# Kernel optimization log

Hardware: AMD Instinct MI355X
Metric: run time of the kernel (lower is better)

Reference implementation:

```python
import jax, jax.numpy as jnp
import numpy as np

NUM_CLASSES = 21
THRESH = 0.5
NEG_POS = 3
VAR0, VAR1 = 0.1, 0.2  # SSD cfg['variance']
B, P, O = 32, 32768, 50


def point_form(boxes):
    # center form (cx,cy,w,h) -> corner form (xmin,ymin,xmax,ymax)
    return jnp.concatenate([boxes[:, :2] - boxes[:, 2:] / 2,
                            boxes[:, :2] + boxes[:, 2:] / 2], axis=1)


def jaccard(box_a, box_b):
    # box_a [A,4], box_b [B,4], corner form -> IoU [A,B]
    max_xy = jnp.minimum(box_a[:, None, 2:], box_b[None, :, 2:])
    min_xy = jnp.maximum(box_a[:, None, :2], box_b[None, :, :2])
    inter = jnp.prod(jnp.clip(max_xy - min_xy, 0.0, None), axis=2)
    area_a = jnp.prod(box_a[:, 2:] - box_a[:, :2], axis=1)[:, None]
    area_b = jnp.prod(box_b[:, 2:] - box_b[:, :2], axis=1)[None, :]
    return inter / (area_a + area_b - inter)


def encode(matched, priors):
    # matched corner form [P,4], priors center form [P,4]
    g_cxcy = ((matched[:, :2] + matched[:, 2:]) / 2 - priors[:, :2]) / (VAR0 * priors[:, 2:])
    g_wh = jnp.log((matched[:, 2:] - matched[:, :2]) / priors[:, 2:]) / VAR1
    return jnp.concatenate([g_cxcy, g_wh], axis=1)


def match_one(truths, labels, priors):
    # truths [O,4] corner, labels [O], priors [P,4] center
    overlaps = jaccard(truths, point_form(priors))          # [O,P]
    best_prior_idx = jnp.argmax(overlaps, axis=1)           # [O]
    best_truth_overlap = jnp.max(overlaps, axis=0)          # [P]
    best_truth_idx = jnp.argmax(overlaps, axis=0)           # [P]
    # ensure every gt matches its best prior
    best_truth_overlap = best_truth_overlap.at[best_prior_idx].set(2.0)
    best_truth_idx = best_truth_idx.at[best_prior_idx].set(jnp.arange(truths.shape[0]))
    matches = truths[best_truth_idx]                        # [P,4]
    conf = (labels[best_truth_idx] + 1.0).astype(jnp.int32)
    conf = jnp.where(best_truth_overlap < THRESH, 0, conf)
    return encode(matches, priors), conf


def setup_inputs() -> dict:
    key = jax.random.key(0)
    k1, k2, k3, k4, k5, k6 = jax.random.split(key, 6)
    loc_data = jax.random.normal(k1, (B, P, 4), dtype=jnp.float32)
    conf_data = jax.random.normal(k2, (B, P, NUM_CLASSES), dtype=jnp.float32)
    # priors in center form: centers in (0,1), sizes in (0.02, 0.5)
    cxy = jax.random.uniform(k3, (P, 2), dtype=jnp.float32)
    wh = jax.random.uniform(k4, (P, 2), dtype=jnp.float32, minval=0.02, maxval=0.5)
    priors = jnp.concatenate([cxy, wh], axis=1)
    # targets: valid corner-form boxes + label
    pts = jax.random.uniform(k5, (B, O, 2, 2), dtype=jnp.float32)
    xymin = pts.min(axis=2)
    xymax = jnp.maximum(pts.max(axis=2), xymin + 0.01)
    labels = jax.random.randint(k6, (B, O), 0, NUM_CLASSES - 1).astype(jnp.float32)
    targets = jnp.concatenate([xymin, xymax, labels[..., None]], axis=-1)
    return {"loc_data": loc_data, "conf_data": conf_data, "priors": priors, "targets": targets}


def reference(loc_data, conf_data, priors, targets):
    truths = targets[..., :4]
    labels = targets[..., 4]
    loc_t, conf_t = jax.vmap(match_one, in_axes=(0, 0, None))(truths, labels, priors)
    loc_t = jax.lax.stop_gradient(loc_t)
    conf_t = jax.lax.stop_gradient(conf_t)

    pos = conf_t > 0                                         # [B,P]
    # localization: smooth-L1, summed over positives
    diff = loc_data - loc_t
    ad = jnp.abs(diff)
    sl1 = jnp.where(ad < 1.0, 0.5 * diff * diff, ad - 0.5)
    loss_l = jnp.sum(sl1 * pos[..., None].astype(sl1.dtype))

    # per-prior softmax CE (logsumexp - true logit)
    lse = jax.nn.logsumexp(conf_data, axis=-1)               # [B,P]
    true_logit = jnp.take_along_axis(conf_data, conf_t[..., None], axis=-1)[..., 0]
    ce = lse - true_logit                                    # [B,P]

    # hard negative mining: rank negatives by CE (pos zeroed out)
    ce_mine = jnp.where(pos, 0.0, ce)
    loss_idx = jnp.argsort(-ce_mine, axis=1)
    idx_rank = jnp.argsort(loss_idx, axis=1)
    num_pos = jnp.sum(pos, axis=1, keepdims=True)            # [B,1]
    num_neg = jnp.clip(NEG_POS * num_pos, None, pos.shape[1] - 1)
    neg = idx_rank < num_neg

    sel = pos | neg
    loss_c = jnp.sum(jnp.where(sel, ce, 0.0))

    N = jnp.sum(num_pos).astype(loss_l.dtype)
    return loss_l / N, loss_c / N
```

## Files before the change

### kernel.cpp

```cpp
#include <hip/hip_runtime.h>
#include <math.h>

#define BB 32
#define PP 32768
#define OO 50
#define NT 25
#define NC 21
#define MPT 4

#define WBINLO (104 << 7)
#define WBINS  2048

typedef unsigned long long u64;
typedef unsigned int u32;
typedef unsigned char u8;

static constexpr u32 HALF_BITS = 0x3F000000u;

static constexpr size_t OFF_WHC   = 0;
static constexpr size_t OFF_WHS   = OFF_WHC  + 4ull*BB*WBINS;
static constexpr size_t OFF_KEYS  = OFF_WHS  + 4ull*BB*WBINS;
static constexpr size_t OFF_NPOS  = OFF_KEYS + 8ull*BB*OO;
static constexpr size_t OFF_DACC  = OFF_NPOS + 128;
static constexpr size_t ZERO_BYTES = OFF_DACC + 8ull*3*BB;
static constexpr size_t OFF_KEY2  = ((ZERO_BYTES + 127) & ~127ull);

__global__ __launch_bounds__(256) void zero_kernel(ulonglong2* __restrict__ dst, size_t n16) {
    size_t i = (size_t)blockIdx.x * 256 + threadIdx.x;
    if (i < n16) dst[i] = make_ulonglong2(0ull, 0ull);
}

static __device__ __forceinline__ float fast_div(float a, float b) {
    return a * __builtin_amdgcn_rcpf(b);
}

__global__ __launch_bounds__(256) void match_kernel(
    const float* __restrict__ priors, const float* __restrict__ targets,
    u64* __restrict__ key2, u64* __restrict__ keys)
{
#pragma clang fp contract(off)
    const int b = blockIdx.y;
    const int half = blockIdx.z;
    const int obase = half * NT;
    const int tid = threadIdx.x;
    const int lane = tid & 63, wid = tid >> 6;
    const int wbase = blockIdx.x * (256 * MPT) + wid * (64 * MPT);

    __shared__ float tr[NT * 5];
    __shared__ u64 wkeys[4][NT];
    if (tid < NT * 5) tr[tid] = targets[(size_t)b * OO * 5 + obase * 5 + tid];
    __syncthreads();

    float px1[MPT], py1[MPT], px2[MPT], py2[MPT], area_p[MPT];
#pragma unroll
    for (int s = 0; s < MPT; ++s) {
        int p = wbase + s * 64 + lane;
        float4 pr = *(const float4*)(priors + (size_t)p * 4);
        px1[s] = pr.x - pr.z * 0.5f; py1[s] = pr.y - pr.w * 0.5f;
        px2[s] = pr.x + pr.z * 0.5f; py2[s] = pr.y + pr.w * 0.5f;
        area_p[s] = (px2[s] - px1[s]) * (py2[s] - py1[s]);
    }

    float bestv[MPT]; int besto[MPT];
#pragma unroll
    for (int s = 0; s < MPT; ++s) { bestv[s] = -1.0f; besto[s] = 0; }

    for (int o = 0; o < NT; ++o) {
        float tx1 = tr[o*5+0], ty1 = tr[o*5+1], tx2 = tr[o*5+2], ty2 = tr[o*5+3];
        float area_t = (tx2 - tx1) * (ty2 - ty1);
        float iou[MPT];
#pragma unroll
        for (int s = 0; s < MPT; ++s) {
            float ix1 = fmaxf(tx1, px1[s]), iy1 = fmaxf(ty1, py1[s]);
            float ix2 = fminf(tx2, px2[s]), iy2 = fminf(ty2, py2[s]);
            float dx = fmaxf(ix2 - ix1, 0.0f), dy = fmaxf(iy2 - iy1, 0.0f);
            float inter = dx * dy;
            iou[s] = fast_div(inter, (area_t + area_p[s]) - inter);
            if (iou[s] > bestv[s]) { bestv[s] = iou[s]; besto[s] = o; }
        }
        float mv = fmaxf(fmaxf(iou[0], iou[1]), fmaxf(iou[2], iou[3]));
        for (int m = 1; m < 64; m <<= 1)
            mv = fmaxf(mv, __shfl_xor(mv, m, 64));
        u64 b0 = __ballot(iou[0] == mv);
        u64 b1 = __ballot(iou[1] == mv);
        u64 b2 = __ballot(iou[2] == mv);
        u64 b3 = __ballot(iou[3] == mv);
        if (lane == 0) {
            int s, l;
            if      (b0) { s = 0; l = __ffsll(b0) - 1; }
            else if (b1) { s = 1; l = __ffsll(b1) - 1; }
            else if (b2) { s = 2; l = __ffsll(b2) - 1; }
            else if (b3) { s = 3; l = __ffsll(b3) - 1; }
            else         { s = 0; l = 0; }
            u32 wp = (u32)(wbase + s * 64 + l);
            wkeys[wid][o] = ((u64)__float_as_uint(mv) << 32) | (u64)(0xFFFFFFFFu - wp);
        }
    }
#pragma unroll
    for (int s = 0; s < MPT; ++s) {
        int p = wbase + s * 64 + lane;
        u64 key = ((u64)__float_as_uint(bestv[s]) << 32)
                | (u64)(u32)(49 - (obase + besto[s]));
        key2[((size_t)half * BB + b) * PP + p] = key;
    }
    __syncthreads();
    if (tid < NT) {
        u64 k0 = wkeys[0][tid];
        for (int w = 1; w < 4; ++w) { u64 kw = wkeys[w][tid]; if (kw > k0) k0 = kw; }
        atomicMax(&keys[b * OO + obase + tid], k0);
    }
}

static __device__ __forceinline__ u32 top16bits(float v) {
    u32 u = __float_as_uint(v);
    return (v > 0.0f) ? u : 0u;
}

static __device__ __forceinline__ u64 umax64(u64 a, u64 b) { return a > b ? a : b; }

#define EL(k) ((((k) & 3) == 0) ? v[(k) >> 2].x : \
               (((k) & 3) == 1) ? v[(k) >> 2].y : \
               (((k) & 3) == 2) ? v[(k) >> 2].z : v[(k) >> 2].w)

__global__ __launch_bounds__(256) void score_kernel(
    const float* __restrict__ loc, const float* __restrict__ conf,
    const float* __restrict__ priors, const float* __restrict__ targets,
    const u64* __restrict__ key2, const u64* __restrict__ keys,
    int* __restrict__ npos, double* __restrict__ dacc,
    u32* __restrict__ whc, float* __restrict__ whs)
{
    const int b = blockIdx.y;
    const int tid = threadIdx.x;
    const int p = blockIdx.x * 1024 + tid * 4;
    __shared__ float tr[OO * 5];
    __shared__ u32 fp[OO];
    __shared__ __align__(16) u32 hh[WBINS];
    __shared__ __align__(16) float hs[WBINS];
    if (tid < OO * 5) tr[tid] = targets[(size_t)b * OO * 5 + tid];
    if (tid < OO) fp[tid] = 0xFFFFFFFFu - (u32)(keys[b * OO + tid] & 0xFFFFFFFFull);
#pragma unroll
    for (int j = 0; j < WBINS / 256; ++j) { hh[j * 256 + tid] = 0; hs[j * 256 + tid] = 0.0f; }
    __syncthreads();

    ulonglong2 a01 = *(const ulonglong2*)(key2 + (size_t)b * PP + p);
    ulonglong2 a23 = *(const ulonglong2*)(key2 + (size_t)b * PP + p + 2);
    ulonglong2 c01 = *(const ulonglong2*)(key2 + ((size_t)BB + b) * PP + p);
    ulonglong2 c23 = *(const ulonglong2*)(key2 + ((size_t)BB + b) * PP + p + 2);
    const u64 kk[4] = {umax64(a01.x, c01.x), umax64(a01.y, c01.y),
                       umax64(a23.x, c23.x), umax64(a23.y, c23.y)};

    int fo[4] = {-1, -1, -1, -1};
    for (int o = 0; o < OO; ++o) {
        u32 fpo = fp[o];
#pragma unroll
        for (int r = 0; r < 4; ++r) if (fpo == (u32)(p + r)) fo[r] = o;
    }

    const float4* cp = (const float4*)(conf + ((size_t)b * PP + p) * NC);
    float4 v[21];
    float cev[4];
    double l_l = 0.0, pce = 0.0; int np_ = 0;

#pragma unroll
    for (int r = 0; r < 4; ++r) {
        const int jlo = (r == 0) ? 0 : ((21 * (r - 1) + 20) / 4 + 1);
        const int jhi = (21 * r + 20) / 4;
#pragma unroll
        for (int j = jlo; j <= jhi; ++j) v[j] = cp[j];

        const u32 hi = (u32)(kk[r] >> 32);
        const u32 lo = (u32)kk[r];
        const bool forced = fo[r] >= 0;
        const int o = forced ? fo[r] : (int)(49u - lo);
        const bool pos = forced || hi >= HALF_BITS;
        const int conft = pos ? (int)(tr[o * 5 + 4] + 1.0f) : 0;

        float m = -1e30f;
#pragma unroll
        for (int c = 0; c < NC; ++c) m = fmaxf(m, EL(21 * r + c));
        float s = 0.0f, tl = 0.0f;
#pragma unroll
        for (int c = 0; c < NC; ++c) {
            float xx = EL(21 * r + c);
            s += expf(xx - m);
            if (c == conft) tl = xx;
        }
        float ce = (m + logf(s)) - tl;
        cev[r] = pos ? 0.0f : ce;

        if (pos) {
            np_ += 1; pce += (double)ce;
            float mx1 = tr[o*5+0], my1 = tr[o*5+1], mx2 = tr[o*5+2], my2 = tr[o*5+3];
            float4 pr = *(const float4*)(priors + (size_t)(p + r) * 4);
            float lt0 = ((mx1 + mx2) * 0.5f - pr.x) / (0.1f * pr.z);
            float lt1 = ((my1 + my2) * 0.5f - pr.y) / (0.1f * pr.w);
            float lt2 = logf((mx2 - mx1) / pr.z) / 0.2f;
            float lt3 = logf((my2 - my1) / pr.w) / 0.2f;
            float4 l4 = *(const float4*)(loc + ((size_t)b * PP + p + r) * 4);
            float lpv[4] = {l4.x, l4.y, l4.z, l4.w};
            float lt[4] = {lt0, lt1, lt2, lt3};
#pragma unroll
            for (int i2 = 0; i2 < 4; ++i2) {
                float d = lpv[i2] - lt[i2];
                float ad = fabsf(d);
                l_l += (double)(ad < 1.0f ? 0.5f * d * d : ad - 0.5f);
            }
        }
    }

#pragma unroll
    for (int r = 0; r < 4; ++r) {
        u32 t16 = top16bits(cev[r]) >> 16;
        if (t16 != 0) {
            int widx = ((int)t16 - WBINLO) >> 1;
            widx = widx < 0 ? 0 : (widx > WBINS - 1 ? WBINS - 1 : widx);
            atomicAdd(&hh[widx], 1u);
            atomicAdd(&hs[widx], cev[r]);
        }
    }
    __syncthreads();
#pragma unroll
    for (int j = 0; j < WBINS / 256; ++j) {
        u32 c = hh[j * 256 + tid];
        if (c) {
            atomicAdd(&whc[(size_t)b * WBINS + j * 256 + tid], c);
            atomicAdd(&whs[(size_t)b * WBINS + j * 256 + tid], hs[j * 256 + tid]);
        }
    }
    __syncthreads();
    double* rl = (double*)hh;
    double* rc = (double*)hs;
    int*    rn = (int*)(hh + 1024);
    rl[tid] = l_l; rc[tid] = pce; rn[tid] = np_;
    __syncthreads();
    for (int s2 = 128; s2 > 0; s2 >>= 1) {
        if (tid < s2) { rl[tid] += rl[tid+s2]; rc[tid] += rc[tid+s2]; rn[tid] += rn[tid+s2]; }
        __syncthreads();
    }
    if (tid == 0) {
        atomicAdd(&dacc[b], rl[0]);
        atomicAdd(&dacc[BB + b], rc[0]);
        atomicAdd(&npos[b], rn[0]);
    }
}

__global__ __launch_bounds__(256) void selwin_kernel(
    const u32* __restrict__ whc, const float* __restrict__ whs,
    const int* __restrict__ npos, double* __restrict__ dacc)
{
    const int b = blockIdx.x, tid = threadIdx.x;
    const int lane = tid & 63, wid = tid >> 6;
    int k = npos[b] * 3; if (k > PP - 1) k = PP - 1;
    if (k <= 0) return;
    const u32* hc = whc + (size_t)b * WBINS;
    const float* hsg = whs + (size_t)b * WBINS;

    __shared__ u32 ccnt_[WBINS / 256]; __shared__ float csum_[WBINS / 256];
    __shared__ u32 ct[256]; __shared__ float fs[256];
    __shared__ int s_cT; __shared__ u32 s_aboveC; __shared__ float s_aboveS;
    __shared__ u32 sT;

    for (int c = wid; c < WBINS / 256; c += 4) {
        u32 cnt = 0; float sm = 0.0f;
#pragma unroll
        for (int q = 0; q < 4; ++q) {
            int idx = c * 256 + q * 64 + lane;
            cnt += hc[idx];
            sm  += hsg[idx];
        }
        for (int m = 1; m < 64; m <<= 1) {
            cnt += __shfl_xor(cnt, m, 64);
            sm  += __shfl_xor(sm, m, 64);
        }
        if (lane == 0) { ccnt_[c] = cnt; csum_[c] = sm; }
    }
    if (tid == 0) sT = 0;
    __syncthreads();
    if (tid == 0) {
        u32 cum = 0; float scum = 0.0f; int cT = -1; u32 aboveC = 0; float aboveS = 0.0f;
        for (int c = WBINS / 256 - 1; c >= 0; --c) {
            if (cum + ccnt_[c] >= (u32)k) { cT = c; aboveC = cum; aboveS = scum; break; }
            cum += ccnt_[c]; scum += csum_[c];
        }
        s_cT = cT; s_aboveC = aboveC; s_aboveS = aboveS;
        if (cT < 0) dacc[2 * BB + b] = (double)scum;
    }
    __syncthreads();
    const int cT = s_cT;
    if (cT < 0) return;
    const u32 aboveC = s_aboveC; const float aboveS = s_aboveS;

    const u32 myc = hc[cT * 256 + tid];
    const float mys = hsg[cT * 256 + tid];
    ct[tid] = myc; fs[tid] = mys;
    __syncthreads();
    for (int off = 1; off < 256; off <<= 1) {
        u32 a1 = (tid + off < 256) ? ct[tid + off] : 0;
        float a2 = (tid + off < 256) ? fs[tid + off] : 0.0f;
        __syncthreads();
        ct[tid] += a1; fs[tid] += a2;
        __syncthreads();
    }
    if (aboveC + ct[tid] >= (u32)k) atomicMax(&sT, (u32)tid);
    __syncthreads();
    const int T = (int)sT;
    if (tid == T) {
        u32 aboveBinC = aboveC + ((T < 255) ? ct[T + 1] : 0);
        float aboveBinS = aboveS + ((T < 255) ? fs[T + 1] : 0.0f);
        int k2 = k - (int)aboveBinC;
        double avg = (double)mys / (double)myc;
        dacc[2 * BB + b] = (double)aboveBinS + (double)k2 * avg;
    }
}

__global__ void finalize_kernel(const int* __restrict__ npos,
                                const double* __restrict__ dacc, float* __restrict__ out) {
    if (threadIdx.x == 0 && blockIdx.x == 0) {
        double N = 0.0, ll = 0.0, lc = 0.0;
        for (int b = 0; b < BB; ++b) {
            N += (double)npos[b];
            ll += dacc[b];
            lc += dacc[BB + b] + dacc[2 * BB + b];
        }
        out[0] = (float)(ll / N);
        out[1] = (float)(lc / N);
    }
}

extern "C" void kernel_launch(void* const* d_in, const int* in_sizes, int n_in,
                              void* d_out, int out_size, void* d_ws, size_t ws_size,
                              hipStream_t stream) {
    const float* loc     = (const float*)d_in[0];
    const float* conf    = (const float*)d_in[1];
    const float* priors  = (const float*)d_in[2];
    const float* targets = (const float*)d_in[3];
    char* ws = (char*)d_ws;
    u32*    whc   = (u32*)   (ws + OFF_WHC);
    float*  whs   = (float*) (ws + OFF_WHS);
    u64*    keys  = (u64*)   (ws + OFF_KEYS);
    int*    npos  = (int*)   (ws + OFF_NPOS);
    double* dacc  = (double*)(ws + OFF_DACC);
    u64*    key2  = (u64*)   (ws + OFF_KEY2);
    float*  out   = (float*)d_out;

    const size_t n16 = ZERO_BYTES / 16;
    zero_kernel<<<(unsigned)((n16 + 255) / 256), 256, 0, stream>>>((ulonglong2*)ws, n16);
    match_kernel<<<dim3(PP / (256 * MPT), BB, 2), 256, 0, stream>>>(priors, targets, key2, keys);
    score_kernel<<<dim3(PP / 1024, BB), 256, 0, stream>>>(loc, conf, priors, targets, key2, keys, npos, dacc, whc, whs);
    selwin_kernel<<<BB, 256, 0, stream>>>(whc, whs, npos, dacc);
    finalize_kernel<<<1, 64, 0, stream>>>(npos, dacc, out);
}
```

Before: 98.62 us.

## Fuse zeroing into match, replace atomics with partials, merge tail kernels

```diff
diff --git a/kernel.cpp b/kernel.cpp
--- a/kernel.cpp
+++ b/kernel.cpp
@@ -6,71 +6,73 @@
 #define OO 50
 #define NT 25
 #define NC 21
-#define MPT 4
 
 #define WBINLO (104 << 7)
 #define WBINS  2048
 
 typedef unsigned long long u64;
 typedef unsigned int u32;
-typedef unsigned char u8;
 
 static constexpr u32 HALF_BITS = 0x3F000000u;
 
 static constexpr size_t OFF_WHC   = 0;
 static constexpr size_t OFF_WHS   = OFF_WHC  + 4ull*BB*WBINS;
-static constexpr size_t OFF_KEYS  = OFF_WHS  + 4ull*BB*WBINS;
-static constexpr size_t OFF_NPOS  = OFF_KEYS + 8ull*BB*OO;
+static constexpr size_t OFF_NPOS  = OFF_WHS  + 4ull*BB*WBINS;
 static constexpr size_t OFF_DACC  = OFF_NPOS + 128;
 static constexpr size_t ZERO_BYTES = OFF_DACC + 8ull*3*BB;
-static constexpr size_t OFF_KEY2  = ((ZERO_BYTES + 127) & ~127ull);
-
-__global__ __launch_bounds__(256) void zero_kernel(ulonglong2* __restrict__ dst, size_t n16) {
-    size_t i = (size_t)blockIdx.x * 256 + threadIdx.x;
-    if (i < n16) dst[i] = make_ulonglong2(0ull, 0ull);
-}
+static constexpr size_t OFF_KPART = ((ZERO_BYTES + 127) & ~127ull);
+static constexpr size_t OFF_KEY2  = OFF_KPART + 8ull*BB*OO*64;
 
 static __device__ __forceinline__ float fast_div(float a, float b) {
     return a * __builtin_amdgcn_rcpf(b);
 }
+static __device__ __forceinline__ u32 top16bits(float v) {
+    u32 u = __float_as_uint(v);
+    return (v > 0.0f) ? u : 0u;
+}
+static __device__ __forceinline__ u64 umax64(u64 a, u64 b) { return a > b ? a : b; }
 
 __global__ __launch_bounds__(256) void match_kernel(
     const float* __restrict__ priors, const float* __restrict__ targets,
-    u64* __restrict__ key2, u64* __restrict__ keys)
+    u64* __restrict__ key2, u64* __restrict__ kpart, ulonglong2* __restrict__ zbase)
 {
-#pragma clang fp contract(off)
     const int b = blockIdx.y;
     const int half = blockIdx.z;
     const int obase = half * NT;
     const int tid = threadIdx.x;
     const int lane = tid & 63, wid = tid >> 6;
-    const int wbase = blockIdx.x * (256 * MPT) + wid * (64 * MPT);
+    const int chunk = blockIdx.x;
+    const int p = chunk * 1024 + tid * 4;
+
+    if (b == 0 && half == 0) {
+        for (size_t i = (size_t)chunk * 256 + tid; i < ZERO_BYTES / 16; i += 32 * 256)
+            zbase[i] = make_ulonglong2(0ull, 0ull);
+    }
 
     __shared__ float tr[NT * 5];
     __shared__ u64 wkeys[4][NT];
     if (tid < NT * 5) tr[tid] = targets[(size_t)b * OO * 5 + obase * 5 + tid];
     __syncthreads();
 
-    float px1[MPT], py1[MPT], px2[MPT], py2[MPT], area_p[MPT];
-#pragma unroll
-    for (int s = 0; s < MPT; ++s) {
-        int p = wbase + s * 64 + lane;
-        float4 pr = *(const float4*)(priors + (size_t)p * 4);
+    float px1[4], py1[4], px2[4], py2[4], area_p[4];
+#pragma unroll
+    for (int s = 0; s < 4; ++s) {
+        float4 pr = *(const float4*)(priors + (size_t)(p + s) * 4);
         px1[s] = pr.x - pr.z * 0.5f; py1[s] = pr.y - pr.w * 0.5f;
         px2[s] = pr.x + pr.z * 0.5f; py2[s] = pr.y + pr.w * 0.5f;
         area_p[s] = (px2[s] - px1[s]) * (py2[s] - py1[s]);
     }
 
-    float bestv[MPT]; int besto[MPT];
-#pragma unroll
-    for (int s = 0; s < MPT; ++s) { bestv[s] = -1.0f; besto[s] = 0; }
+    float bestv[4]; int besto[4];
+#pragma unroll
+    for (int s = 0; s < 4; ++s) { bestv[s] = -1.0f; besto[s] = 0; }
 
     for (int o = 0; o < NT; ++o) {
         float tx1 = tr[o*5+0], ty1 = tr[o*5+1], tx2 = tr[o*5+2], ty2 = tr[o*5+3];
         float area_t = (tx2 - tx1) * (ty2 - ty1);
-        float iou[MPT];
-#pragma unroll
-        for (int s = 0; s < MPT; ++s) {
+        float iou[4];
+#pragma unroll
+        for (int s = 0; s < 4; ++s) {
             float ix1 = fmaxf(tx1, px1[s]), iy1 = fmaxf(ty1, py1[s]);
             float ix2 = fminf(tx2, px2[s]), iy2 = fminf(ty2, py2[s]);
             float dx = fmaxf(ix2 - ix1, 0.0f), dy = fmaxf(iy2 - iy1, 0.0f);
@@ -78,45 +80,35 @@
             iou[s] = fast_div(inter, (area_t + area_p[s]) - inter);
             if (iou[s] > bestv[s]) { bestv[s] = iou[s]; besto[s] = o; }
         }
-        float mv = fmaxf(fmaxf(iou[0], iou[1]), fmaxf(iou[2], iou[3]));
+        float tmax = iou[0]; int ts = 0;
+#pragma unroll
+        for (int s = 1; s < 4; ++s) if (iou[s] > tmax) { tmax = iou[s]; ts = s; }
+        float mv = tmax;
         for (int m = 1; m < 64; m <<= 1)
             mv = fmaxf(mv, __shfl_xor(mv, m, 64));
-        u64 b0 = __ballot(iou[0] == mv);
-        u64 b1 = __ballot(iou[1] == mv);
-        u64 b2 = __ballot(iou[2] == mv);
-        u64 b3 = __ballot(iou[3] == mv);
-        if (lane == 0) {
-            int s, l;
-            if      (b0) { s = 0; l = __ffsll(b0) - 1; }
-            else if (b1) { s = 1; l = __ffsll(b1) - 1; }
-            else if (b2) { s = 2; l = __ffsll(b2) - 1; }
-            else if (b3) { s = 3; l = __ffsll(b3) - 1; }
-            else         { s = 0; l = 0; }
-            u32 wp = (u32)(wbase + s * 64 + l);
-            wkeys[wid][o] = ((u64)__float_as_uint(mv) << 32) | (u64)(0xFFFFFFFFu - wp);
-        }
-    }
-#pragma unroll
-    for (int s = 0; s < MPT; ++s) {
-        int p = wbase + s * 64 + lane;
-        u64 key = ((u64)__float_as_uint(bestv[s]) << 32)
-                | (u64)(u32)(49 - (obase + besto[s]));
-        key2[((size_t)half * BB + b) * PP + p] = key;
+        u64 bm = __ballot(tmax == mv);
+        if (lane == (int)(__ffsll((long long)bm) - 1))
+            wkeys[wid][o] = ((u64)__float_as_uint(mv) << 32)
+                          | (u64)(0xFFFFFFFFu - (u32)(p + ts));
+    }
+
+    {
+        u64 k0 = ((u64)__float_as_uint(bestv[0]) << 32) | (u64)(u32)(49 - (obase + besto[0]));
+        u64 k1 = ((u64)__float_as_uint(bestv[1]) << 32) | (u64)(u32)(49 - (obase + besto[1]));
+        u64 k2 = ((u64)__float_as_uint(bestv[2]) << 32) | (u64)(u32)(49 - (obase + besto[2]));
+        u64 k3 = ((u64)__float_as_uint(bestv[3]) << 32) | (u64)(u32)(49 - (obase + besto[3]));
+        u64* dst = key2 + ((size_t)half * BB + b) * PP + p;
+        *(ulonglong2*)dst = make_ulonglong2(k0, k1);
+        *(ulonglong2*)(dst + 2) = make_ulonglong2(k2, k3);
     }
     __syncthreads();
     if (tid < NT) {
         u64 k0 = wkeys[0][tid];
-        for (int w = 1; w < 4; ++w) { u64 kw = wkeys[w][tid]; if (kw > k0) k0 = kw; }
-        atomicMax(&keys[b * OO + obase + tid], k0);
-    }
-}
-
-static __device__ __forceinline__ u32 top16bits(float v) {
-    u32 u = __float_as_uint(v);
-    return (v > 0.0f) ? u : 0u;
-}
-
-static __device__ __forceinline__ u64 umax64(u64 a, u64 b) { return a > b ? a : b; }
+#pragma unroll
+        for (int w = 1; w < 4; ++w) k0 = umax64(k0, wkeys[w][tid]);
+        kpart[((size_t)b * OO + obase + tid) * 64 + chunk * 2 + half] = k0;
+    }
+}
 
 #define EL(k) ((((k) & 3) == 0) ? v[(k) >> 2].x : \
                (((k) & 3) == 1) ? v[(k) >> 2].y : \
@@ -125,7 +117,7 @@
 __global__ __launch_bounds__(256) void score_kernel(
     const float* __restrict__ loc, const float* __restrict__ conf,
     const float* __restrict__ priors, const float* __restrict__ targets,
-    const u64* __restrict__ key2, const u64* __restrict__ keys,
+    const u64* __restrict__ key2, const u64* __restrict__ kpart,
     int* __restrict__ npos, double* __restrict__ dacc,
     u32* __restrict__ whc, float* __restrict__ whs)
 {
@@ -137,7 +129,12 @@
     __shared__ __align__(16) u32 hh[WBINS];
     __shared__ __align__(16) float hs[WBINS];
     if (tid < OO * 5) tr[tid] = targets[(size_t)b * OO * 5 + tid];
-    if (tid < OO) fp[tid] = 0xFFFFFFFFu - (u32)(keys[b * OO + tid] & 0xFFFFFFFFull);
+    if (tid < OO) {
+        const u64* kp = kpart + ((size_t)b * OO + tid) * 64;
+        u64 k0 = kp[0];
+        for (int c = 1; c < 64; ++c) k0 = umax64(k0, kp[c]);
+        fp[tid] = 0xFFFFFFFFu - (u32)(k0 & 0xFFFFFFFFull);
+    }
 #pragma unroll
     for (int j = 0; j < WBINS / 256; ++j) { hh[j * 256 + tid] = 0; hs[j * 256 + tid] = 0.0f; }
     __syncthreads();
@@ -244,78 +241,79 @@
     }
 }
 
-__global__ __launch_bounds__(256) void selwin_kernel(
+__global__ __launch_bounds__(256) void tail_kernel(
     const u32* __restrict__ whc, const float* __restrict__ whs,
-    const int* __restrict__ npos, double* __restrict__ dacc)
+    const int* __restrict__ npos, double* __restrict__ dacc,
+    float* __restrict__ out)
 {
-    const int b = blockIdx.x, tid = threadIdx.x;
+    const int tid = threadIdx.x;
     const int lane = tid & 63, wid = tid >> 6;
-    int k = npos[b] * 3; if (k > PP - 1) k = PP - 1;
-    if (k <= 0) return;
-    const u32* hc = whc + (size_t)b * WBINS;
-    const float* hsg = whs + (size_t)b * WBINS;
-
     __shared__ u32 ccnt_[WBINS / 256]; __shared__ float csum_[WBINS / 256];
     __shared__ u32 ct[256]; __shared__ float fs[256];
     __shared__ int s_cT; __shared__ u32 s_aboveC; __shared__ float s_aboveS;
     __shared__ u32 sT;
 
-    for (int c = wid; c < WBINS / 256; c += 4) {
-        u32 cnt = 0; float sm = 0.0f;
-#pragma unroll
-        for (int q = 0; q < 4; ++q) {
-            int idx = c * 256 + q * 64 + lane;
-            cnt += hc[idx];
-            sm  += hsg[idx];
-        }
-        for (int m = 1; m < 64; m <<= 1) {
-            cnt += __shfl_xor(cnt, m, 64);
-            sm  += __shfl_xor(sm, m, 64);
-        }
-        if (lane == 0) { ccnt_[c] = cnt; csum_[c] = sm; }
-    }
-    if (tid == 0) sT = 0;
+    for (int b = 0; b < BB; ++b) {
+        int k = npos[b] * 3; if (k > PP - 1) k = PP - 1;
+        if (k > 0) {
+            const u32* hc = whc + (size_t)b * WBINS;
+            const float* hsg = whs + (size_t)b * WBINS;
+            for (int c = wid; c < WBINS / 256; c += 4) {
+                u32 cnt = 0; float sm = 0.0f;
+#pragma unroll
+                for (int q = 0; q < 4; ++q) {
+                    int idx = c * 256 + q * 64 + lane;
+                    cnt += hc[idx];
+                    sm  += hsg[idx];
+                }
+                for (int m = 1; m < 64; m <<= 1) {
+                    cnt += __shfl_xor(cnt, m, 64);
+                    sm  += __shfl_xor(sm, m, 64);
+                }
+                if (lane == 0) { ccnt_[c] = cnt; csum_[c] = sm; }
+            }
+            if (tid == 0) sT = 0;
+            __syncthreads();
+            if (tid == 0) {
+                u32 cum = 0; float scum = 0.0f; int cT = -1; u32 aC = 0; float aS = 0.0f;
+                for (int c = WBINS / 256 - 1; c >= 0; --c) {
+                    if (cum + ccnt_[c] >= (u32)k) { cT = c; aC = cum; aS = scum; break; }
+                    cum += ccnt_[c]; scum += csum_[c];
+                }
+                s_cT = cT; s_aboveC = aC; s_aboveS = aS;
+                if (cT < 0) dacc[2 * BB + b] = (double)scum;
+            }
+            __syncthreads();
+            const int cT = s_cT;
+            if (cT >= 0) {
+                const u32 aboveC = s_aboveC; const float aboveS = s_aboveS;
+                const u32 myc = hc[cT * 256 + tid];
+                const float mys = hsg[cT * 256 + tid];
+                ct[tid] = myc; fs[tid] = mys;
+                __syncthreads();
+                for (int off = 1; off < 256; off <<= 1) {
+                    u32 a1 = (tid + off < 256) ? ct[tid + off] : 0;
+                    float a2 = (tid + off < 256) ? fs[tid + off] : 0.0f;
+                    __syncthreads();
+                    ct[tid] += a1; fs[tid] += a2;
+                    __syncthreads();
+                }
+                if (aboveC + ct[tid] >= (u32)k) atomicMax(&sT, (u32)tid);
+                __syncthreads();
+                const int T = (int)sT;
+                if (tid == T) {
+                    u32 aboveBinC = aboveC + ((T < 255) ? ct[T + 1] : 0);
+                    float aboveBinS = aboveS + ((T < 255) ? fs[T + 1] : 0.0f);
+                    int k2 = k - (int)aboveBinC;
+                    double avg = (double)mys / (double)myc;
+                    dacc[2 * BB + b] = (double)aboveBinS + (double)k2 * avg;
+                }
+            }
+            __syncthreads();
+        }
+    }
     __syncthreads();
     if (tid == 0) {
-        u32 cum = 0; float scum = 0.0f; int cT = -1; u32 aboveC = 0; float aboveS = 0.0f;
-        for (int c = WBINS / 256 - 1; c >= 0; --c) {
-            if (cum + ccnt_[c] >= (u32)k) { cT = c; aboveC = cum; aboveS = scum; break; }
-            cum += ccnt_[c]; scum += csum_[c];
-        }
-        s_cT = cT; s_aboveC = aboveC; s_aboveS = aboveS;
-        if (cT < 0) dacc[2 * BB + b] = (double)scum;
-    }
-    __syncthreads();
-    const int cT = s_cT;
-    if (cT < 0) return;
-    const u32 aboveC = s_aboveC; const float aboveS = s_aboveS;
-
-    const u32 myc = hc[cT * 256 + tid];
-    const float mys = hsg[cT * 256 + tid];
-    ct[tid] = myc; fs[tid] = mys;
-    __syncthreads();
-    for (int off = 1; off < 256; off <<= 1) {
-        u32 a1 = (tid + off < 256) ? ct[tid + off] : 0;
-        float a2 = (tid + off < 256) ? fs[tid + off] : 0.0f;
-        __syncthreads();
-        ct[tid] += a1; fs[tid] += a2;
-        __syncthreads();
-    }
-    if (aboveC + ct[tid] >= (u32)k) atomicMax(&sT, (u32)tid);
-    __syncthreads();
-    const int T = (int)sT;
-    if (tid == T) {
-        u32 aboveBinC = aboveC + ((T < 255) ? ct[T + 1] : 0);
-        float aboveBinS = aboveS + ((T < 255) ? fs[T + 1] : 0.0f);
-        int k2 = k - (int)aboveBinC;
-        double avg = (double)mys / (double)myc;
-        dacc[2 * BB + b] = (double)aboveBinS + (double)k2 * avg;
-    }
-}
-
-__global__ void finalize_kernel(const int* __restrict__ npos,
-                                const double* __restrict__ dacc, float* __restrict__ out) {
-    if (threadIdx.x == 0 && blockIdx.x == 0) {
         double N = 0.0, ll = 0.0, lc = 0.0;
         for (int b = 0; b < BB; ++b) {
             N += (double)npos[b];
@@ -337,16 +335,13 @@
     char* ws = (char*)d_ws;
     u32*    whc   = (u32*)   (ws + OFF_WHC);
     float*  whs   = (float*) (ws + OFF_WHS);
-    u64*    keys  = (u64*)   (ws + OFF_KEYS);
     int*    npos  = (int*)   (ws + OFF_NPOS);
     double* dacc  = (double*)(ws + OFF_DACC);
+    u64*    kpart = (u64*)   (ws + OFF_KPART);
     u64*    key2  = (u64*)   (ws + OFF_KEY2);
     float*  out   = (float*)d_out;
 
-    const size_t n16 = ZERO_BYTES / 16;
-    zero_kernel<<<(unsigned)((n16 + 255) / 256), 256, 0, stream>>>((ulonglong2*)ws, n16);
-    match_kernel<<<dim3(PP / (256 * MPT), BB, 2), 256, 0, stream>>>(priors, targets, key2, keys);
-    score_kernel<<<dim3(PP / 1024, BB), 256, 0, stream>>>(loc, conf, priors, targets, key2, keys, npos, dacc, whc, whs);
-    selwin_kernel<<<BB, 256, 0, stream>>>(whc, whs, npos, dacc);
-    finalize_kernel<<<1, 64, 0, stream>>>(npos, dacc, out);
-}
+    match_kernel<<<dim3(PP / 1024, BB, 2), 256, 0, stream>>>(priors, targets, key2, kpart, (ulonglong2*)ws);
+    score_kernel<<<dim3(PP / 1024, BB), 256, 0, stream>>>(loc, conf, priors, targets, key2, kpart, npos, dacc, whc, whs);
+    tail_kernel<<<1, 256, 0, stream>>>(whc, whs, npos, dacc, out);
+}
```

After: 229.5 us. +132.7%, slower.
